# Optimization experiments

Hardware: AMD Instinct MI355X
Metric: run time of the kernel (lower is better)

Reference implementation:

```python
import jax, jax.numpy as jnp
import numpy as np

B, NQ, NKV = 2, 2048, 2048
QUERY_DIM = 1024
CONTEXT_DIM = 1024
HEADS = 16
DIM_HEAD = 64
INNER = HEADS * DIM_HEAD
SCALE = DIM_HEAD ** -0.5


def setup_inputs() -> dict:
    key = jax.random.key(0)
    ks = jax.random.split(key, 9)
    x = jax.random.normal(ks[0], (B, NQ, QUERY_DIM), dtype=jnp.float32)
    context = jax.random.normal(ks[1], (B, NKV, CONTEXT_DIM), dtype=jnp.float32)
    tgt_mask = jax.random.randint(ks[2], (B, 1, NQ, NKV), 0, 2, dtype=jnp.int32)
    src_mask = jax.random.randint(ks[3], (B, 1, NKV), 0, 2) > 0  # bool [b,1,j]
    w = 0.02
    Wq = jax.random.normal(ks[4], (INNER, QUERY_DIM), dtype=jnp.float32) * w
    Wk = jax.random.normal(ks[5], (INNER, CONTEXT_DIM), dtype=jnp.float32) * w
    Wv = jax.random.normal(ks[6], (INNER, CONTEXT_DIM), dtype=jnp.float32) * w
    Wo = jax.random.normal(ks[7], (QUERY_DIM, INNER), dtype=jnp.float32) * w
    bo = jax.random.normal(ks[8], (QUERY_DIM,), dtype=jnp.float32) * w
    return {"x": x, "context": context, "tgt_mask": tgt_mask, "src_mask": src_mask,
            "Wq": Wq, "Wk": Wk, "Wv": Wv, "Wo": Wo, "bo": bo}


def reference(x, context, tgt_mask, src_mask, Wq, Wk, Wv, Wo, bo):
    b, nq, _ = x.shape
    nkv = context.shape[1]
    # Linear projections (torch Linear: y = x @ W.T), split into heads: b n (h d) -> b h n d
    q = jnp.einsum('bnc,ec->bne', x, Wq).reshape(b, nq, HEADS, DIM_HEAD).transpose(0, 2, 1, 3)
    k = jnp.einsum('bmc,ec->bme', context, Wk).reshape(b, nkv, HEADS, DIM_HEAD).transpose(0, 2, 1, 3)
    v = jnp.einsum('bmc,ec->bme', context, Wv).reshape(b, nkv, HEADS, DIM_HEAD).transpose(0, 2, 1, 3)
    sim = jnp.einsum('bhid,bhjd->bhij', q, k) * SCALE
    neg = -jnp.finfo(sim.dtype).max
    sim = jnp.where(tgt_mask == 0, neg, sim)                 # tgt_mask [b,1,i,j]
    sim = jnp.where(src_mask[:, None, :], sim, neg)          # src_mask [b,1,j] -> [b,1,1,j]
    attn = jax.nn.softmax(sim, axis=-1)
    out = jnp.einsum('bhij,bhjd->bhid', attn, v)
    out = out.transpose(0, 2, 1, 3).reshape(b, nq, INNER)    # b h n d -> b n (h d)
    return jnp.einsum('bne,oe->bno', out, Wo) + bo           # dropout=0 at inference
```

## Files before the change

### kernel.cpp

```cpp
#include <hip/hip_runtime.h>

typedef short short8 __attribute__((ext_vector_type(8)));
typedef float f32x4 __attribute__((ext_vector_type(4)));
typedef float f32x16 __attribute__((ext_vector_type(16)));
typedef unsigned u32x4 __attribute__((ext_vector_type(4)));

#define GLOAD_LDS(src, dst) \
  __builtin_amdgcn_global_load_lds((const __attribute__((address_space(1))) void*)(src), \
                                   (__attribute__((address_space(3))) void*)(dst), 16, 0, 0)

__device__ __forceinline__ unsigned short f2b(float f){
  __bf16 h = (__bf16)f;
  return __builtin_bit_cast(unsigned short, h);
}
__device__ __forceinline__ unsigned pk2(float a, float b){
  unsigned r;
  asm("v_cvt_pk_bf16_f32 %0, %1, %2" : "=v"(r) : "v"(a), "v"(b));
  return r;
}
__device__ __forceinline__ float fexp2(float x){
  return __builtin_amdgcn_exp2f(x);
}
__device__ __forceinline__ float b2f(unsigned short u){
  union { unsigned u; float f; } cv;
  cv.u = ((unsigned)u) << 16;
  return cv.f;
}

__global__ __launch_bounds__(256) void prep(const float* __restrict__ x, const float* __restrict__ ctx,
    const float* __restrict__ wq, const float* __restrict__ wk, const float* __restrict__ wv,
    const float* __restrict__ wo, const int* __restrict__ tgt, const void* __restrict__ srcm,
    unsigned short* __restrict__ xb, unsigned short* __restrict__ cb, unsigned short* __restrict__ wqb,
    unsigned short* __restrict__ wkvb, unsigned short* __restrict__ wob,
    unsigned long long* __restrict__ mp){
  const int blk = blockIdx.x;
  if (blk < 12288){
    const int i = blk * 256 + threadIdx.x;
    const float* src; unsigned short* dst; int so, doff;
    if (i < 1048576)      { src = x;   dst = xb;   so = i;           doff = so; }
    else if (i < 2097152) { src = ctx; dst = cb;   so = i - 1048576; doff = so; }
    else if (i < 2359296) { src = wq;  dst = wqb;  so = i - 2097152; doff = so; }
    else if (i < 2621440) { src = wk;  dst = wkvb; so = i - 2359296; doff = so; }
    else if (i < 2883584) { src = wv;  dst = wkvb; so = i - 2621440; doff = so + 262144; }
    else                  { src = wo;  dst = wob;  so = i - 2883584; doff = so; }
    const float4 v = reinterpret_cast<const float4*>(src)[so];
    ushort4 o;
    o.x = f2b(v.x); o.y = f2b(v.y); o.z = f2b(v.z); o.w = f2b(v.w);
    reinterpret_cast<ushort4*>(dst)[doff] = o;
  } else {
    size_t gt = (size_t)(blk - 12288) * 256 + threadIdx.x;
    int j = (int)(gt & 2047);
    size_t bi = gt >> 11;
    int b = (int)(bi >> 11);
    const int j0 = j & ~255;
    const unsigned wv32 = ((const unsigned*)srcm)[((b * 2048 + j0) >> 2) + (threadIdx.x & 63)];
    const bool u8mode = __ballot(wv32 > 1u) != 0ull;
    bool s;
    if (u8mode) s = ((const unsigned char*)srcm)[b * 2048 + j] != 0;
    else        s = ((const int*)srcm)[b * 2048 + j] != 0;
    bool bit = (tgt[gt] != 0) && s;
    unsigned long long m = __ballot(bit ? 1 : 0);
    if ((threadIdx.x & 63) == 0) mp[gt >> 6] = m;
  }
}

__global__ __launch_bounds__(256) void masktr(const unsigned long long* __restrict__ mp,
                                              unsigned* __restrict__ mpT2){
  const int tile = blockIdx.x * 4 + (threadIdx.x >> 6);
  const int lane = threadIdx.x & 63;
  const int b  = tile >> 10;
  const int it = (tile >> 5) & 31;
  const int jt = tile & 31;
  unsigned long long xv = mp[((size_t)b * 2048 + it * 64 + lane) * 32 + jt];
  const unsigned long long A0 = 0x00000000FFFFFFFFull, A1 = 0x0000FFFF0000FFFFull,
                           A2 = 0x00FF00FF00FF00FFull, A3 = 0x0F0F0F0F0F0F0F0Full,
                           A4 = 0x3333333333333333ull, A5 = 0x5555555555555555ull;
#define TRSTEP(K, A) { \
    unsigned long long y = __shfl_xor(xv, K); \
    xv = (lane & (K)) ? (((y >> (K)) & (A)) | (xv & ~(A))) \
                      : ((xv & (A)) | ((y & (A)) << (K))); }
  TRSTEP(32, A0) TRSTEP(16, A1) TRSTEP(8, A2) TRSTEP(4, A3) TRSTEP(2, A4) TRSTEP(1, A5)
#undef TRSTEP
  unsigned* dst = mpT2 + (((size_t)b * 32 + jt) * 64 + it * 2) * 64 + lane;
  dst[0]  = (unsigned)xv;
  dst[64] = (unsigned)(xv >> 32);
}

#define G_DECLS \
  const int tid = threadIdx.x; \
  const int lane = tid & 63, wid = tid >> 6; \
  const int l15 = lane & 15, l4 = lane >> 4; \
  const int wm = wid >> 1, wn = wid & 1; \
  __shared__ unsigned short lA[3][128 * 32]; \
  __shared__ unsigned short lB[3][128 * 32]; \
  f32x4 acc[4][4] = {}; \
  const int r0 = tid >> 2, q0 = tid & 3; \
  const int r1 = (tid + 256) >> 2; \
  const unsigned short* a0p = A  + (size_t)(m0 + r0) * 1024 + q0 * 8; \
  const unsigned short* a1p = A  + (size_t)(m0 + r1) * 1024 + q0 * 8; \
  const unsigned short* b0p = Bw + (size_t)(n0 + r0) * 1024 + q0 * 8; \
  const unsigned short* b1p = Bw + (size_t)(n0 + r1) * 1024 + q0 * 8; \
  const int d0 = (wid * 64) * 8, d1 = (wid * 64 + 256) * 8;

#define G_STAGE(K0, BUF) { \
    GLOAD_LDS(a0p + (K0), &lA[BUF][d0]); \
    GLOAD_LDS(a1p + (K0), &lA[BUF][d1]); \
    GLOAD_LDS(b0p + (K0), &lB[BUF][d0]); \
    GLOAD_LDS(b1p + (K0), &lB[BUF][d1]); }

#define GCOMPUTE(BR) { \
  short8 af[4], bf[4]; \
  _Pragma("unroll") for (int m = 0; m < 4; m++) \
    af[m] = *reinterpret_cast<const short8*>(&lA[BR][(wm * 64 + m * 16 + l15) * 32 + l4 * 8]); \
  _Pragma("unroll") for (int n = 0; n < 4; n++) \
    bf[n] = *reinterpret_cast<const short8*>(&lB[BR][(wn * 64 + n * 16 + l15) * 32 + l4 * 8]); \
  _Pragma("unroll") for (int m = 0; m < 4; m++) \
    _Pragma("unroll") for (int n = 0; n < 4; n++) \
      acc[m][n] = __builtin_amdgcn_mfma_f32_16x16x32_bf16(af[m], bf[n], acc[m][n], 0, 0, 0); \
}

#define GITER(T, BR, BS, VM) { \
  asm volatile("s_waitcnt vmcnt(" #VM ")\n\ts_barrier" ::: "memory"); \
  if ((T) < 30) G_STAGE(((T) + 2) * 32, BS) \
  GCOMPUTE(BR) \
}

#define G_LOOP \
  G_STAGE(0, 0) \
  G_STAGE(32, 1) \
  for (int u = 0; u < 30; u += 3){ \
    GITER(u, 0, 2, 4) \
    GITER(u + 1, 1, 0, 4) \
    GITER(u + 2, 2, 1, 4) \
  } \
  GITER(30, 0, 2, 4) \
  GITER(31, 1, 0, 0)

__global__ __launch_bounds__(256, 3) void gemm_qkv(const unsigned short* __restrict__ xb,
                                                const unsigned short* __restrict__ cbuf,
                                                const unsigned short* __restrict__ wqb,
                                                const unsigned short* __restrict__ wkvb,
                                                unsigned short* __restrict__ qws,
                                                unsigned short* __restrict__ kws,
                                                unsigned short* __restrict__ vtw){
  const int f = blockIdx.x;
  const unsigned short *A, *Bw;
  int m0, n0, mode;
  if (f < 256){ A = xb;   Bw = wqb;  m0 = (f >> 3) * 128;  n0 = (f & 7) * 128;  mode = 0; }
  else { const int g = f - 256;
         A = cbuf; Bw = wkvb; m0 = (g >> 4) * 128;  n0 = (g & 15) * 128; mode = 1; }
  G_DECLS
  G_LOOP

  const int eb = n0 + wn * 64;
  const int mb = m0 + wm * 64 + l4 * 4;
  #pragma unroll
  for (int n = 0; n < 4; n++){
    const int e = eb + n * 16 + l15;
    #pragma unroll
    for (int m = 0; m < 4; m++){
      const int mm = mb + m * 16;
      if (mode == 0){
        const int h = e >> 6, d = e & 63;
        #pragma unroll
        for (int r = 0; r < 4; r++){
          const int row = mm + r, b = row >> 11, nn = row & 2047;
          qws[(((size_t)b * 16 + h) * 2048 + nn) * 64 + d] = f2b(acc[m][n][r] * 0.18033688011112042f);
        }
      } else {
        if (e < 1024){
          const int h = e >> 6, d = e & 63;
          #pragma unroll
          for (int r = 0; r < 4; r++){
            const int row = mm + r, b = row >> 11, nn = row & 2047;
            kws[(((size_t)b * 16 + h) * 2048 + nn) * 64 + d] = f2b(acc[m][n][r]);
          }
        } else {
          const int ee = e - 1024, h = ee >> 6, d = ee & 63;
          const int b = mm >> 11, nn = mm & 2047;
          ushort4 pk;
          pk.x = f2b(acc[m][n][0]); pk.y = f2b(acc[m][n][1]);
          pk.z = f2b(acc[m][n][2]); pk.w = f2b(acc[m][n][3]);
          *reinterpret_cast<ushort4*>(&vtw[(((size_t)b * 16 + h) * 64 + d) * 2048 + nn]) = pk;
        }
      }
    }
  }
}

__global__ __launch_bounds__(256, 3) void gemm_o(const unsigned short* __restrict__ A,
                                              const unsigned short* __restrict__ Bw,
                                              float* __restrict__ fout,
                                              const float* __restrict__ bias){
  const int m0 = blockIdx.y * 128, n0 = blockIdx.x * 128;
  G_DECLS
  G_LOOP

  const int eb = n0 + wn * 64;
  const int mb = m0 + wm * 64 + l4 * 4;
  #pragma unroll
  for (int n = 0; n < 4; n++){
    const int e = eb + n * 16 + l15;
    const float bv = bias[e];
    #pragma unroll
    for (int m = 0; m < 4; m++){
      const int mm = mb + m * 16;
      #pragma unroll
      for (int r = 0; r < 4; r++)
        fout[(size_t)(mm + r) * 1024 + e] = acc[m][n][r] + bv;
    }
  }
}

#define A_STAGE(T, BUF) { \
    const int jj = jbase + (T) * 64; \
    GLOAD_LDS(kb + (size_t)(jj + sr0) * 64 + sc0 * 8, &lK[BUF][dk0]); \
    GLOAD_LDS(kb + (size_t)(jj + sr1) * 64 + sc1 * 8, &lK[BUF][dk1]); \
    GLOAD_LDS(vb + (size_t)sr0 * 2048 + jj + sc0 * 8, &lV[BUF][dk0]); \
    GLOAD_LDS(vb + (size_t)sr1 * 2048 + jj + sc1 * 8, &lV[BUF][dk1]); }

#define A_COMPUTE(BR, T) { \
  const char* kbase = (const char*)lK[BR]; \
  f32x16 st0 = {}, st1 = {}; \
  __builtin_amdgcn_s_setprio(1); \
  _Pragma("unroll") for (int ks = 0; ks < 4; ks++){ \
    const short8 a0 = *reinterpret_cast<const short8*>(kbase + (((l31) * 128 + ks * 32 + hi * 16) ^ sw)); \
    st0 = __builtin_amdgcn_mfma_f32_32x32x16_bf16(a0, qf[ks], st0, 0, 0, 0); \
  } \
  _Pragma("unroll") for (int ks = 0; ks < 4; ks++){ \
    const short8 a1 = *reinterpret_cast<const short8*>(kbase + (((l31 + 32) * 128 + ks * 32 + hi * 16) ^ sw)); \
    st1 = __builtin_amdgcn_mfma_f32_32x32x16_bf16(a1, qf[ks], st1, 0, 0, 0); \
  } \
  __builtin_amdgcn_s_setprio(0); \
  const unsigned* mt = mt0 + (size_t)(T) * 4096; \
  _Pragma("unroll") for (int r = 0; r < 16; r++){ \
    const int dj = (r & 3) + 8 * (r >> 2); \
    const unsigned long long mk0 = (unsigned long long)mt[dj] | ((unsigned long long)mt[dj + 4] << 32); \
    const unsigned long long mk1 = (unsigned long long)mt[dj + 32] | ((unsigned long long)mt[dj + 36] << 32); \
    float v0, v1; \
    asm("v_cndmask_b32 %0, %1, %2, %3" : "=v"(v0) : "v"(negv), "v"((float)st0[r]), "s"(mk0)); \
    asm("v_cndmask_b32 %0, %1, %2, %3" : "=v"(v1) : "v"(negv), "v"((float)st1[r]), "s"(mk1)); \
    st0[r] = fexp2(v0); \
    st1[r] = fexp2(v1); \
  } \
  float s8[8]; \
  _Pragma("unroll") for (int i = 0; i < 8; i++) \
    s8[i] = (st0[i] + st0[i + 8]) + (st1[i] + st1[i + 8]); \
  l_i += ((s8[0] + s8[1]) + (s8[2] + s8[3])) + ((s8[4] + s8[5]) + (s8[6] + s8[7])); \
  const char* vbase = (const char*)lV[BR]; \
  _Pragma("unroll") for (int ks = 0; ks < 4; ks++){ \
    unsigned A0, B0, A1, B1; \
    if (ks < 2){ \
      A0 = pk2(st0[8 * ks + 0], st0[8 * ks + 1]); \
      B0 = pk2(st0[8 * ks + 2], st0[8 * ks + 3]); \
      A1 = pk2(st0[8 * ks + 4], st0[8 * ks + 5]); \
      B1 = pk2(st0[8 * ks + 6], st0[8 * ks + 7]); \
    } else { \
      A0 = pk2(st1[8 * (ks - 2) + 0], st1[8 * (ks - 2) + 1]); \
      B0 = pk2(st1[8 * (ks - 2) + 2], st1[8 * (ks - 2) + 3]); \
      A1 = pk2(st1[8 * (ks - 2) + 4], st1[8 * (ks - 2) + 5]); \
      B1 = pk2(st1[8 * (ks - 2) + 6], st1[8 * (ks - 2) + 7]); \
    } \
    asm("v_permlane32_swap_b32 %0, %1" : "+v"(A0), "+v"(A1)); \
    asm("v_permlane32_swap_b32 %0, %1" : "+v"(B0), "+v"(B1)); \
    const short8 pf = __builtin_bit_cast(short8, (u32x4){A0, B0, A1, B1}); \
    __builtin_amdgcn_s_setprio(1); \
    const short8 va0 = *reinterpret_cast<const short8*>(vbase + (((l31) * 128 + ks * 32 + hi * 16) ^ sw)); \
    o0_ = __builtin_amdgcn_mfma_f32_32x32x16_bf16(va0, pf, o0_, 0, 0, 0); \
    const short8 va1 = *reinterpret_cast<const short8*>(vbase + (((l31 + 32) * 128 + ks * 32 + hi * 16) ^ sw)); \
    o1_ = __builtin_amdgcn_mfma_f32_32x32x16_bf16(va1, pf, o1_, 0, 0, 0); \
    __builtin_amdgcn_s_setprio(0); \
  } \
}

__global__ __launch_bounds__(256, 4) void attn(const unsigned short* __restrict__ qw,
                                            const unsigned short* __restrict__ kw,
                                            const unsigned short* __restrict__ vtw,
                                            const unsigned* __restrict__ mpT2,
                                            unsigned short* __restrict__ opb,
                                            float* __restrict__ lsum){
  const int f = blockIdx.x;
  const int xcd = f & 7, slot = f >> 3;
  const int bh = xcd * 4 + (slot & 3);
  const int r2 = slot >> 2;
  const int qtile = r2 >> 1, kvh = r2 & 1;
  const int b = bh >> 4;
  const int qbase = qtile * 128;
  const int jbase = kvh * 1024;
  const int tid = threadIdx.x, wid = tid >> 6, lane = tid & 63;
  const int l31 = lane & 31, hi = lane >> 5;
  __shared__ unsigned short lK[2][64 * 64];
  __shared__ unsigned short lV[2][64 * 64];

  const int qrow = qbase + wid * 32 + l31;
  const unsigned short* qp = qw + ((size_t)bh * 2048 + qrow) * 64 + hi * 8;
  short8 qf[4];
  #pragma unroll
  for (int ks = 0; ks < 4; ks++)
    qf[ks] = *reinterpret_cast<const short8*>(qp + ks * 16);

  const int sr0 = tid >> 3,          sc0 = (tid & 7) ^ (sr0 & 7);
  const int sr1 = (tid + 256) >> 3,  sc1 = ((tid + 256) & 7) ^ (sr1 & 7);
  const unsigned short* kb = kw  + (size_t)bh * 2048 * 64;
  const unsigned short* vb = vtw + (size_t)bh * 64 * 2048;
  const int dk0 = (wid * 64) * 8, dk1 = (wid * 64 + 256) * 8;

  const int widu = __builtin_amdgcn_readfirstlane(wid);
  const int qw32 = qtile * 4 + widu;
  const unsigned* mt0 = mpT2 + (((size_t)b * 32 + kvh * 16) * 64 + qw32) * 64;

  float l_i = 0.f;
  f32x16 o0_ = {}, o1_ = {};
  const int sw = (l31 & 7) << 4;
  const float negv = -3.0e38f;

  A_STAGE(0, 0)
  __syncthreads();

  int cb_ = 0;
  for (int t = 0; t < 16; t++){
    if (t < 15) A_STAGE(t + 1, cb_ ^ 1)
    A_COMPUTE(cb_, t)
    if (t < 15) __syncthreads();
    cb_ ^= 1;
  }

  l_i += __shfl_xor(l_i, 32);
  const int row = wid * 32 + l31;
  const int pidx = (bh * 16 + qtile) * 2 + kvh;
  unsigned short* opr = opb + (size_t)pidx * 8192 + row * 64;
  #pragma unroll
  for (int rq = 0; rq < 4; rq++){
    uint2 w0, w1;
    w0.x = pk2(o0_[rq * 4 + 0], o0_[rq * 4 + 1]); w0.y = pk2(o0_[rq * 4 + 2], o0_[rq * 4 + 3]);
    w1.x = pk2(o1_[rq * 4 + 0], o1_[rq * 4 + 1]); w1.y = pk2(o1_[rq * 4 + 2], o1_[rq * 4 + 3]);
    *reinterpret_cast<uint2*>(opr + rq * 8 + hi * 4)      = w0;
    *reinterpret_cast<uint2*>(opr + 32 + rq * 8 + hi * 4) = w1;
  }
  if (!hi)
    lsum[pidx * 128 + row] = l_i;
}

__global__ __launch_bounds__(256) void combine(const unsigned short* __restrict__ opb,
                                               const float* __restrict__ lsum,
                                               unsigned short* __restrict__ ao){
  const int g = blockIdx.x;
  const int bh = g >> 4, qtile = g & 15;
  const int b = bh >> 4, h = bh & 15;
  const int row = threadIdx.x >> 1;
  const int dh = (threadIdx.x & 1) * 32;
  const float l = lsum[(g * 2 + 0) * 128 + row] + lsum[(g * 2 + 1) * 128 + row];
  const float inv = 1.f / l;
  const unsigned short* p0 = opb + ((size_t)(g * 2 + 0)) * 8192 + row * 64 + dh;
  const unsigned short* p1 = opb + ((size_t)(g * 2 + 1)) * 8192 + row * 64 + dh;
  unsigned short* o = ao + ((size_t)b * 2048 + qtile * 128 + row) * 1024 + h * 64 + dh;
  #pragma unroll
  for (int i = 0; i < 4; i++){
    short8 v0 = *reinterpret_cast<const short8*>(p0 + i * 8);
    short8 v1 = *reinterpret_cast<const short8*>(p1 + i * 8);
    ushort4 wa, wb;
    #pragma unroll
    for (int e = 0; e < 4; e++){
      ((unsigned short*)&wa)[e] = f2b((b2f((unsigned short)v0[e]) + b2f((unsigned short)v1[e])) * inv);
      ((unsigned short*)&wb)[e] = f2b((b2f((unsigned short)v0[e + 4]) + b2f((unsigned short)v1[e + 4])) * inv);
    }
    reinterpret_cast<ushort4*>(o)[i * 2]     = wa;
    reinterpret_cast<ushort4*>(o)[i * 2 + 1] = wb;
  }
}

extern "C" void kernel_launch(void* const* d_in, const int* in_sizes, int n_in,
                              void* d_out, int out_size, void* d_ws, size_t ws_size,
                              hipStream_t stream){
  const float* x   = (const float*)d_in[0];
  const float* ctx = (const float*)d_in[1];
  const int*   tgt = (const int*)d_in[2];
  const void*  src = d_in[3];
  const float* Wq  = (const float*)d_in[4];
  const float* Wk  = (const float*)d_in[5];
  const float* Wv  = (const float*)d_in[6];
  const float* Wo  = (const float*)d_in[7];
  const float* bo  = (const float*)d_in[8];
  float* out = (float*)d_out;

  char* w = (char*)d_ws;
  unsigned short* xb   = (unsigned short*)(w);
  unsigned short* cb   = (unsigned short*)(w + (8u << 20));
  unsigned short* wqb  = (unsigned short*)(w + (16u << 20));
  unsigned short* wkvb = (unsigned short*)(w + (18u << 20));
  unsigned short* wob  = (unsigned short*)(w + (22u << 20));
  unsigned short* qws  = (unsigned short*)(w + (24u << 20));
  unsigned short* kws  = (unsigned short*)(w + (32u << 20));
  unsigned short* vtw  = (unsigned short*)(w + (40u << 20));
  unsigned long long* mp = (unsigned long long*)(w + (48u << 20));
  unsigned short* opb  = (unsigned short*)(w + (50u << 20));
  unsigned* mpT2 = (unsigned*)(w + (16u << 20));
  float* lsum = (float*)(w + (8u << 20));
  unsigned short* ao = (unsigned short*)(w);

  prep<<<12288 + 32768, 256, 0, stream>>>(x, ctx, Wq, Wk, Wv, Wo, tgt, src,
                                          xb, cb, wqb, wkvb, wob, mp);
  gemm_qkv<<<768, 256, 0, stream>>>(xb, cb, wqb, wkvb, qws, kws, vtw);
  masktr<<<512, 256, 0, stream>>>(mp, mpT2);
  attn<<<1024, 256, 0, stream>>>(qws, kws, vtw, mpT2, opb, lsum);
  combine<<<512, 256, 0, stream>>>(opb, lsum, ao);
  gemm_o<<<dim3(8, 32), 256, 0, stream>>>(ao, wob, out, bo);
}
```

Baseline: 151.0 us.

## Fuse mask packing and bit transpose into prep kernel, grid-stride bf16 casts

The separate masktr kernel is removed. The prep kernel now builds each 64x64 mask tile directly: one wave reads 64 rows of tgt_mask, ballots each row, and transposes the bits in registers before writing mpT2. This drops the intermediate mp buffer and one kernel launch. The bf16 conversion part becomes a grid-stride loop over 2048 blocks instead of 12288, and mpT2 moves to its own workspace region so it no longer overlaps the wqb buffer.

New measurement: 139.5 us. -7.6%, faster.

```diff
diff --git a/kernel.cpp b/kernel.cpp
--- a/kernel.cpp
+++ b/kernel.cpp
@@ -32,58 +32,58 @@
     const float* __restrict__ wo, const int* __restrict__ tgt, const void* __restrict__ srcm,
     unsigned short* __restrict__ xb, unsigned short* __restrict__ cb, unsigned short* __restrict__ wqb,
     unsigned short* __restrict__ wkvb, unsigned short* __restrict__ wob,
-    unsigned long long* __restrict__ mp){
+    unsigned* __restrict__ mpT2){
   const int blk = blockIdx.x;
-  if (blk < 12288){
-    const int i = blk * 256 + threadIdx.x;
-    const float* src; unsigned short* dst; int so, doff;
-    if (i < 1048576)      { src = x;   dst = xb;   so = i;           doff = so; }
-    else if (i < 2097152) { src = ctx; dst = cb;   so = i - 1048576; doff = so; }
-    else if (i < 2359296) { src = wq;  dst = wqb;  so = i - 2097152; doff = so; }
-    else if (i < 2621440) { src = wk;  dst = wkvb; so = i - 2359296; doff = so; }
-    else if (i < 2883584) { src = wv;  dst = wkvb; so = i - 2621440; doff = so + 262144; }
-    else                  { src = wo;  dst = wob;  so = i - 2883584; doff = so; }
-    const float4 v = reinterpret_cast<const float4*>(src)[so];
-    ushort4 o;
-    o.x = f2b(v.x); o.y = f2b(v.y); o.z = f2b(v.z); o.w = f2b(v.w);
-    reinterpret_cast<ushort4*>(dst)[doff] = o;
+  if (blk < 2048){
+    for (int i = blk * 256 + threadIdx.x; i < 3145728; i += 2048 * 256){
+      const float* src; unsigned short* dst; int so, doff;
+      if (i < 1048576)      { src = x;   dst = xb;   so = i;           doff = so; }
+      else if (i < 2097152) { src = ctx; dst = cb;   so = i - 1048576; doff = so; }
+      else if (i < 2359296) { src = wq;  dst = wqb;  so = i - 2097152; doff = so; }
+      else if (i < 2621440) { src = wk;  dst = wkvb; so = i - 2359296; doff = so; }
+      else if (i < 2883584) { src = wv;  dst = wkvb; so = i - 2621440; doff = so + 262144; }
+      else                  { src = wo;  dst = wob;  so = i - 2883584; doff = so; }
+      const float4 v = reinterpret_cast<const float4*>(src)[so];
+      ushort4 o;
+      o.x = f2b(v.x); o.y = f2b(v.y); o.z = f2b(v.z); o.w = f2b(v.w);
+      reinterpret_cast<ushort4*>(dst)[doff] = o;
+    }
   } else {
-    size_t gt = (size_t)(blk - 12288) * 256 + threadIdx.x;
-    int j = (int)(gt & 2047);
-    size_t bi = gt >> 11;
-    int b = (int)(bi >> 11);
-    const int j0 = j & ~255;
-    const unsigned wv32 = ((const unsigned*)srcm)[((b * 2048 + j0) >> 2) + (threadIdx.x & 63)];
-    const bool u8mode = __ballot(wv32 > 1u) != 0ull;
-    bool s;
-    if (u8mode) s = ((const unsigned char*)srcm)[b * 2048 + j] != 0;
-    else        s = ((const int*)srcm)[b * 2048 + j] != 0;
-    bool bit = (tgt[gt] != 0) && s;
-    unsigned long long m = __ballot(bit ? 1 : 0);
-    if ((threadIdx.x & 63) == 0) mp[gt >> 6] = m;
-  }
-}
-
-__global__ __launch_bounds__(256) void masktr(const unsigned long long* __restrict__ mp,
-                                              unsigned* __restrict__ mpT2){
-  const int tile = blockIdx.x * 4 + (threadIdx.x >> 6);
-  const int lane = threadIdx.x & 63;
-  const int b  = tile >> 10;
-  const int it = (tile >> 5) & 31;
-  const int jt = tile & 31;
-  unsigned long long xv = mp[((size_t)b * 2048 + it * 64 + lane) * 32 + jt];
-  const unsigned long long A0 = 0x00000000FFFFFFFFull, A1 = 0x0000FFFF0000FFFFull,
-                           A2 = 0x00FF00FF00FF00FFull, A3 = 0x0F0F0F0F0F0F0F0Full,
-                           A4 = 0x3333333333333333ull, A5 = 0x5555555555555555ull;
+    const int t = (blk - 2048) * 4 + (threadIdx.x >> 6);
+    const int lane = threadIdx.x & 63;
+    const int bb = t >> 10, it = (t >> 5) & 31, jt = t & 31;
+    const unsigned dw = ((const unsigned*)srcm)[((bb * 2048 + jt * 64) >> 2) + (lane & 15)];
+    const bool u8mode = __ballot(dw > 1u) != 0ull;
+    bool sbit;
+    if (u8mode) sbit = ((const unsigned char*)srcm)[bb * 2048 + jt * 64 + lane] != 0;
+    else        sbit = ((const int*)srcm)[bb * 2048 + jt * 64 + lane] != 0;
+    unsigned long long xv = 0ull;
+    const int* tg = tgt + ((size_t)(bb * 2048 + it * 64)) * 2048 + jt * 64 + lane;
+    #pragma unroll
+    for (int rb = 0; rb < 64; rb += 8){
+      int v[8];
+      #pragma unroll
+      for (int r = 0; r < 8; r++)
+        v[r] = tg[(size_t)(rb + r) * 2048];
+      #pragma unroll
+      for (int r = 0; r < 8; r++){
+        const unsigned long long wbits = __ballot(sbit && (v[r] != 0));
+        xv = (lane == rb + r) ? wbits : xv;
+      }
+    }
+    const unsigned long long A0 = 0x00000000FFFFFFFFull, A1 = 0x0000FFFF0000FFFFull,
+                             A2 = 0x00FF00FF00FF00FFull, A3 = 0x0F0F0F0F0F0F0F0Full,
+                             A4 = 0x3333333333333333ull, A5 = 0x5555555555555555ull;
 #define TRSTEP(K, A) { \
     unsigned long long y = __shfl_xor(xv, K); \
     xv = (lane & (K)) ? (((y >> (K)) & (A)) | (xv & ~(A))) \
                       : ((xv & (A)) | ((y & (A)) << (K))); }
-  TRSTEP(32, A0) TRSTEP(16, A1) TRSTEP(8, A2) TRSTEP(4, A3) TRSTEP(2, A4) TRSTEP(1, A5)
+    TRSTEP(32, A0) TRSTEP(16, A1) TRSTEP(8, A2) TRSTEP(4, A3) TRSTEP(2, A4) TRSTEP(1, A5)
 #undef TRSTEP
-  unsigned* dst = mpT2 + (((size_t)b * 32 + jt) * 64 + it * 2) * 64 + lane;
-  dst[0]  = (unsigned)xv;
-  dst[64] = (unsigned)(xv >> 32);
+    unsigned* dst = mpT2 + (((size_t)bb * 32 + jt) * 64 + it * 2) * 64 + lane;
+    dst[0]  = (unsigned)xv;
+    dst[64] = (unsigned)(xv >> 32);
+  }
 }
 
 #define G_DECLS \
@@ -392,16 +392,14 @@
   unsigned short* qws  = (unsigned short*)(w + (24u << 20));
   unsigned short* kws  = (unsigned short*)(w + (32u << 20));
   unsigned short* vtw  = (unsigned short*)(w + (40u << 20));
-  unsigned long long* mp = (unsigned long long*)(w + (48u << 20));
+  unsigned* mpT2       = (unsigned*)(w + (48u << 20));
   unsigned short* opb  = (unsigned short*)(w + (50u << 20));
-  unsigned* mpT2 = (unsigned*)(w + (16u << 20));
   float* lsum = (float*)(w + (8u << 20));
   unsigned short* ao = (unsigned short*)(w);
 
-  prep<<<12288 + 32768, 256, 0, stream>>>(x, ctx, Wq, Wk, Wv, Wo, tgt, src,
-                                          xb, cb, wqb, wkvb, wob, mp);
+  prep<<<2560, 256, 0, stream>>>(x, ctx, Wq, Wk, Wv, Wo, tgt, src,
+                                 xb, cb, wqb, wkvb, wob, mpT2);
   gemm_qkv<<<768, 256, 0, stream>>>(xb, cb, wqb, wkvb, qws, kws, vtw);
-  masktr<<<512, 256, 0, stream>>>(mp, mpT2);
   attn<<<1024, 256, 0, stream>>>(qws, kws, vtw, mpT2, opb, lsum);
   combine<<<512, 256, 0, stream>>>(opb, lsum, ao);
   gemm_o<<<dim3(8, 32), 256, 0, stream>>>(ao, wob, out, bo);
```
